# Performance work log

Hardware: AMD Instinct MI355X
Metric: run time of the kernel (lower is better)

The kernel has to match this reference:

```python
import jax, jax.numpy as jnp
import numpy as np


def setup_inputs() -> dict:
    key = jax.random.key(0)
    ks = jax.random.split(key, 12)
    B, T, S, H, I = 32, 32, 400, 1024, 1024
    s = 0.02  # weight init scale
    return {
        "input_": jax.random.normal(ks[0], (B, T, I), jnp.float32),
        "h0": jax.random.normal(ks[1], (B, H), jnp.float32),
        "c0": jax.random.normal(ks[2], (B, H), jnp.float32),
        "h_attn0": jax.random.normal(ks[3], (B, H), jnp.float32),
        "encoder_hy": jax.random.normal(ks[4], (S, B, H), jnp.float32),
        "past_attn": jax.random.uniform(ks[5], (B, S), jnp.float32),
        "W_ih": jax.random.normal(ks[6], (4 * H, I + H), jnp.float32) * s,
        "W_hh": jax.random.normal(ks[7], (4 * H, H), jnp.float32) * s,
        "b_ih": jnp.zeros((4 * H,), jnp.float32),
        "b_hh": jnp.zeros((4 * H,), jnp.float32),
        "W_attn": jax.random.normal(ks[8], (H, H), jnp.float32) * s,
        "W_out": jax.random.normal(ks[9], (H, 2 * H), jnp.float32) * s,
    }


def _decode(input_, h0, c0, h_attn0, encoder_hy, W_ih, W_hh, b_ih, b_hh, W_attn, W_out):
    # encoder_hy: [S, B, H] -> enhy: [B, S, H]
    enhy = jnp.transpose(encoder_hy, (1, 0, 2))
    # attn_in(enhy) is time-invariant (linear, fixed enhy): hoist out of the loop
    enhy_new = jnp.einsum("bsh,gh->bsg", enhy, W_attn)  # [B, S, H]
    xs = jnp.transpose(input_, (1, 0, 2))  # [T, B, I] (batch_first)

    def step(carry, x_k):
        h, c, h_attn = carry
        x = jnp.concatenate([x_k, h_attn], axis=1)  # [B, I+H]
        gates = x @ W_ih.T + b_ih + h @ W_hh.T + b_hh  # [B, 4H]
        i, f, g, o = jnp.split(gates, 4, axis=1)  # torch LSTMCell gate order
        i = jax.nn.sigmoid(i)
        f = jax.nn.sigmoid(f)
        g = jnp.tanh(g)
        o = jax.nn.sigmoid(o)
        c = f * c + i * g
        h = o * jnp.tanh(c)
        # luong_general: attn = bmm(attn_in(enhy), dehy)
        attn = jax.nn.softmax(jnp.einsum("bsh,bh->bs", enhy_new, h), axis=1)
        ctx = jnp.einsum("bs,bsh->bh", attn, enhy)
        h_attn = jnp.tanh(jnp.concatenate([ctx, h], axis=1) @ W_out.T)
        return (h, c, h_attn), (h_attn, attn)

    (h, c, h_attn), (outs, attns) = jax.lax.scan(step, (h0, c0, h_attn0), xs)
    output = jnp.transpose(outs, (1, 0, 2))  # [B, T, H] (batch_first)
    return output, h, c, h_attn, attns  # attns: [T, B, S]


def reference(input_, h0, c0, h_attn0, encoder_hy, past_attn,
              W_ih, W_hh, b_ih, b_hh, W_attn, W_out):
    output, h, c, h_attn, out_attn = _decode(
        input_, h0, c0, h_attn0, encoder_hy, W_ih, W_hh, b_ih, b_hh, W_attn, W_out)
    # coverage='none': past_attn passes through unchanged; loss_cv stays 0.0
    return output, h, c, h_attn, out_attn, past_attn, jnp.float32(0.0)
```

## Files before the change

kernel.cpp:

```cpp
#include <hip/hip_runtime.h>
#include <hip/hip_bf16.h>

using u16 = unsigned short;
typedef __attribute__((ext_vector_type(8))) short bf16x8;
typedef __attribute__((ext_vector_type(4))) float f32x4;
typedef __attribute__((ext_vector_type(4))) u16 u16x4;


__device__ __forceinline__ float bf2f(u16 u){ union{unsigned int i; float f;} v; v.i = ((unsigned int)u)<<16; return v.f; }
__device__ __forceinline__ u16 f2bf(float f){ __hip_bfloat16 h = __float2bfloat16(f); return *reinterpret_cast<u16*>(&h); }
struct HL { u16 h, l; };
__device__ __forceinline__ HL split1(float f){
  HL r; r.h = f2bf(f); r.l = f2bf(f - bf2f(r.h)); return r;
}
__device__ __forceinline__ f32x4 mfma16(bf16x8 a, bf16x8 b, f32x4 c){ return __builtin_amdgcn_mfma_f32_16x16x32_bf16(a,b,c,0,0,0); }


__global__ __launch_bounds__(256) void cast_wih_k(const float* __restrict__ Wih,
    u16* __restrict__ Wxh, u16* __restrict__ Wxl, u16* __restrict__ Wrh, u16* __restrict__ Wrl){
  int v = blockIdx.x*256 + threadIdx.x;
  if (v >= (4096*2048)/4) return;
  int flat = v*4; int j = flat >> 11; int k = flat & 2047;
  float4 f = *(const float4*)(Wih + flat);
  HL s0 = split1(f.x), s1 = split1(f.y), s2 = split1(f.z), s3 = split1(f.w);
  u16x4 h, l;
  h[0]=s0.h; h[1]=s1.h; h[2]=s2.h; h[3]=s3.h;
  l[0]=s0.l; l[1]=s1.l; l[2]=s2.l; l[3]=s3.l;
  if (k < 1024){
    *(u16x4*)(Wxh + (size_t)j*1024 + k) = h;
    *(u16x4*)(Wxl + (size_t)j*1024 + k) = l;
  } else {
    *(u16x4*)(Wrh + (size_t)j*2048 + (k-1024)) = h;
    *(u16x4*)(Wrl + (size_t)j*2048 + (k-1024)) = l;
  }
}

__global__ __launch_bounds__(256) void cast_whh_k(const float* __restrict__ Whh,
    u16* __restrict__ Wrh, u16* __restrict__ Wrl){
  int v = blockIdx.x*256 + threadIdx.x;
  if (v >= (4096*1024)/4) return;
  int flat = v*4; int j = flat >> 10; int k = flat & 1023;
  float4 f = *(const float4*)(Whh + flat);
  HL s0 = split1(f.x), s1 = split1(f.y), s2 = split1(f.z), s3 = split1(f.w);
  u16x4 h, l;
  h[0]=s0.h; h[1]=s1.h; h[2]=s2.h; h[3]=s3.h;
  l[0]=s0.l; l[1]=s1.l; l[2]=s2.l; l[3]=s3.l;
  *(u16x4*)(Wrh + (size_t)j*2048 + 1024 + k) = h;
  *(u16x4*)(Wrl + (size_t)j*2048 + 1024 + k) = l;
}

__global__ __launch_bounds__(256) void cast_split_k(const float* __restrict__ src,
    u16* __restrict__ dh, u16* __restrict__ dl, int n4){
  int v = blockIdx.x*256 + threadIdx.x;
  if (v >= n4) return;
  float4 f = *(const float4*)(src + (size_t)v*4);
  HL s0 = split1(f.x), s1 = split1(f.y), s2 = split1(f.z), s3 = split1(f.w);
  u16x4 h, l;
  h[0]=s0.h; h[1]=s1.h; h[2]=s2.h; h[3]=s3.h;
  l[0]=s0.l; l[1]=s1.l; l[2]=s2.l; l[3]=s3.l;
  *(u16x4*)(dh + (size_t)v*4) = h;
  *(u16x4*)(dl + (size_t)v*4) = l;
}

__global__ __launch_bounds__(256) void cast_x_k(const float* __restrict__ inp,
    u16* __restrict__ Xh, u16* __restrict__ Xl){
  int v = blockIdx.x*256 + threadIdx.x;
  if (v >= (1024*1024)/4) return;
  int flat = v*4; int m = flat >> 10; int k = flat & 1023;
  int t = m >> 5, b = m & 31;
  float4 f = *(const float4*)(inp + ((size_t)(b*32 + t) << 10) + k);
  HL s0 = split1(f.x), s1 = split1(f.y), s2 = split1(f.z), s3 = split1(f.w);
  u16x4 h, l;
  h[0]=s0.h; h[1]=s1.h; h[2]=s2.h; h[3]=s3.h;
  l[0]=s0.l; l[1]=s1.l; l[2]=s2.l; l[3]=s3.l;
  *(u16x4*)(Xh + flat) = h;
  *(u16x4*)(Xl + flat) = l;
}

__global__ __launch_bounds__(256) void watsplit_k(const float* __restrict__ Wattn,
    u16* __restrict__ Wth, u16* __restrict__ Wtl){
  __shared__ float t[32][33];
  int gx = blockIdx.x, cx = blockIdx.y;
  int ty = threadIdx.x >> 5, tx = threadIdx.x & 31;
  #pragma unroll
  for (int i=0;i<4;++i){
    int g = gx*32 + ty + i*8;
    t[ty+i*8][tx] = Wattn[(size_t)g*1024 + cx*32 + tx];
  }
  __syncthreads();
  #pragma unroll
  for (int i=0;i<4;++i){
    int c = cx*32 + ty + i*8;
    HL s = split1(t[tx][ty+i*8]);
    Wth[(size_t)c*1024 + gx*32 + tx] = s.h;
    Wtl[(size_t)c*1024 + gx*32 + tx] = s.l;
  }
}

__global__ __launch_bounds__(256) void cast_encb_k(const float* __restrict__ enc,
    u16* __restrict__ encb){
  int v = blockIdx.x*256 + threadIdx.x;
  if (v >= (400*32*1024)/8) return;
  size_t flat = (size_t)v*8;
  int c = flat & 1023; int rem = flat >> 10;
  int b = rem & 31, s = rem >> 5;
  float4 f0 = *(const float4*)(enc + flat);
  float4 f1 = *(const float4*)(enc + flat + 4);
  u16x4 h0, h1;
  h0[0]=f2bf(f0.x); h0[1]=f2bf(f0.y); h0[2]=f2bf(f0.z); h0[3]=f2bf(f0.w);
  h1[0]=f2bf(f1.x); h1[1]=f2bf(f1.y); h1[2]=f2bf(f1.z); h1[3]=f2bf(f1.w);
  u16* dst = encb + ((size_t)b*400 + s)*1024 + c;
  *(u16x4*)dst = h0;
  *(u16x4*)(dst+4) = h1;
}

__global__ __launch_bounds__(256) void init_misc_k(const float* __restrict__ h0, const float* __restrict__ c0,
    const float* __restrict__ ha0, const float* __restrict__ past,
    u16* __restrict__ Zh0, u16* __restrict__ Zl0, float* __restrict__ cbuf,
    float* __restrict__ out_past, float* __restrict__ out_loss){
  int idx = blockIdx.x*256 + threadIdx.x;
  if (idx < 65536){
    int b = idx >> 11, col = idx & 2047;
    float v = (col < 1024) ? ha0[b*1024 + col] : h0[b*1024 + col - 1024];
    HL s = split1(v);
    Zh0[idx] = s.h; Zl0[idx] = s.l;
  } else if (idx < 65536 + 32768){
    int i = idx - 65536; cbuf[i] = c0[i];
  } else if (idx < 65536 + 32768 + 12800){
    int i = idx - 98304; out_past[i] = past[i];
  } else if (idx == 65536 + 32768 + 12800){
    out_loss[0] = 0.f;
  }
}

__global__ __launch_bounds__(256) void gemm128_bias_k(
    const u16* __restrict__ Ah, const u16* __restrict__ Al,
    const u16* __restrict__ Bh, const u16* __restrict__ Bl, float* __restrict__ C,
    const float* __restrict__ bias0, const float* __restrict__ bias1, int M, int N, int K)
{
  __shared__ __align__(16) u16 Ash[4096], Asl[4096], Bsh[4096], Bsl[4096];
  const int tid = threadIdx.x;
  const int lane = tid & 63, w = tid >> 6;
  const int wm = w >> 1, wn = w & 1;
  const int m0 = blockIdx.y * 128, n0 = blockIdx.x * 128;
  const int r = lane & 15, q = lane >> 4;

  f32x4 acc[4][4];
  #pragma unroll
  for (int i=0;i<4;i++)
    #pragma unroll
    for (int j=0;j<4;j++) acc[i][j] = (f32x4){0.f,0.f,0.f,0.f};

  const int NT = K >> 5;
  const int srow = tid >> 2;
  const int skp  = (tid & 3) * 8;
  bf16x8 rah0, rah1, ral0, ral1, rbh0, rbh1, rbl0, rbl1;

  {
    size_t ao = (size_t)(m0 + srow) * K + skp;
    size_t bo = (size_t)(n0 + srow) * K + skp;
    rah0 = *(const bf16x8*)(Ah + ao);  rah1 = *(const bf16x8*)(Ah + ao + (size_t)64*K);
    ral0 = *(const bf16x8*)(Al + ao);  ral1 = *(const bf16x8*)(Al + ao + (size_t)64*K);
    rbh0 = *(const bf16x8*)(Bh + bo);  rbh1 = *(const bf16x8*)(Bh + bo + (size_t)64*K);
    rbl0 = *(const bf16x8*)(Bl + bo);  rbl1 = *(const bf16x8*)(Bl + bo + (size_t)64*K);
  }

  for (int kt = 0; kt < NT; ++kt){
    __syncthreads();
    *(bf16x8*)(Ash + tid*8)        = rah0;
    *(bf16x8*)(Ash + 2048 + tid*8) = rah1;
    *(bf16x8*)(Asl + tid*8)        = ral0;
    *(bf16x8*)(Asl + 2048 + tid*8) = ral1;
    *(bf16x8*)(Bsh + tid*8)        = rbh0;
    *(bf16x8*)(Bsh + 2048 + tid*8) = rbh1;
    *(bf16x8*)(Bsl + tid*8)        = rbl0;
    *(bf16x8*)(Bsl + 2048 + tid*8) = rbl1;
    __syncthreads();
    if (kt + 1 < NT){
      size_t ao = (size_t)(m0 + srow) * K + (kt+1)*32 + skp;
      size_t bo = (size_t)(n0 + srow) * K + (kt+1)*32 + skp;
      rah0 = *(const bf16x8*)(Ah + ao);  rah1 = *(const bf16x8*)(Ah + ao + (size_t)64*K);
      ral0 = *(const bf16x8*)(Al + ao);  ral1 = *(const bf16x8*)(Al + ao + (size_t)64*K);
      rbh0 = *(const bf16x8*)(Bh + bo);  rbh1 = *(const bf16x8*)(Bh + bo + (size_t)64*K);
      rbl0 = *(const bf16x8*)(Bl + bo);  rbl1 = *(const bf16x8*)(Bl + bo + (size_t)64*K);
    }
    bf16x8 afh[4], afl[4], bfh[4], bfl[4];
    #pragma unroll
    for (int mf=0; mf<4; ++mf){
      int off = (wm*64 + mf*16 + r)*32 + q*8;
      afh[mf] = *(const bf16x8*)(Ash + off);
      afl[mf] = *(const bf16x8*)(Asl + off);
    }
    #pragma unroll
    for (int nf=0; nf<4; ++nf){
      int off = (wn*64 + nf*16 + r)*32 + q*8;
      bfh[nf] = *(const bf16x8*)(Bsh + off);
      bfl[nf] = *(const bf16x8*)(Bsl + off);
    }
    #pragma unroll
    for (int mf=0; mf<4; ++mf)
      #pragma unroll
      for (int nf=0; nf<4; ++nf){
        acc[mf][nf] = mfma16(afh[mf], bfh[nf], acc[mf][nf]);
        acc[mf][nf] = mfma16(afh[mf], bfl[nf], acc[mf][nf]);
        acc[mf][nf] = mfma16(afl[mf], bfh[nf], acc[mf][nf]);
      }
  }

  #pragma unroll
  for (int mf=0; mf<4; ++mf)
    #pragma unroll
    for (int nf=0; nf<4; ++nf)
      #pragma unroll
      for (int rr=0; rr<4; ++rr){
        int row = m0 + wm*64 + mf*16 + q*4 + rr;
        int col = n0 + wn*64 + nf*16 + r;
        C[(size_t)row*N + col] = acc[mf][nf][rr] + bias0[col] + bias1[col];
      }
}


__global__ __launch_bounds__(512) void rec_cell_k(
    const u16* __restrict__ Zh, const u16* __restrict__ Zl,
    const u16* __restrict__ Wh, const u16* __restrict__ Wl,
    const float* __restrict__ gX, float* __restrict__ cbuf,
    u16* __restrict__ Znh, u16* __restrict__ Znl,
    u16* __restrict__ Zoh, u16* __restrict__ Zol,
    float* __restrict__ out_h, float* __restrict__ out_c, int last)
{
  __shared__ float red[8][512];
  __shared__ float gsum[512];
  const int tid = threadIdx.x, lane = tid & 63, w = tid >> 6;
  const int j4 = blockIdx.x;
  const int r = lane & 15, q = lane >> 4;
  const int k0 = w*256;

  f32x4 acc0 = (f32x4){0,0,0,0}, acc1 = (f32x4){0,0,0,0};
  const size_t aoff = (size_t)r*2048 + k0 + q*8;
  const size_t boff = (size_t)((r>>2)*1024 + j4*4 + (r&3))*2048 + k0 + q*8;
  #pragma unroll
  for (int kt = 0; kt < 8; ++kt){
    bf16x8 a0h = *(const bf16x8*)(Zh + aoff + kt*32);
    bf16x8 a0l = *(const bf16x8*)(Zl + aoff + kt*32);
    bf16x8 a1h = *(const bf16x8*)(Zh + aoff + (size_t)16*2048 + kt*32);
    bf16x8 a1l = *(const bf16x8*)(Zl + aoff + (size_t)16*2048 + kt*32);
    bf16x8 bh  = *(const bf16x8*)(Wh + boff + kt*32);
    bf16x8 bl  = *(const bf16x8*)(Wl + boff + kt*32);
    acc0 = mfma16(a0h, bh, acc0);
    acc0 = mfma16(a0h, bl, acc0);
    acc0 = mfma16(a0l, bh, acc0);
    acc1 = mfma16(a1h, bh, acc1);
    acc1 = mfma16(a1h, bl, acc1);
    acc1 = mfma16(a1l, bh, acc1);
  }
  #pragma unroll
  for (int rr=0; rr<4; ++rr){
    red[w][(q*4+rr)*16 + r]        = acc0[rr];
    red[w][256 + (q*4+rr)*16 + r]  = acc1[rr];
  }
  __syncthreads();
  {
    float v = 0.f;
    #pragma unroll
    for (int w2=0; w2<8; ++w2) v += red[w2][tid];
    gsum[tid] = v;
  }
  __syncthreads();
  if (tid < 128){
    int b = tid >> 2, c = tid & 3;
    int j = j4*4 + c;
    float gs[4];
    #pragma unroll
    for (int g=0; g<4; ++g)
      gs[g] = gsum[b*16 + g*4 + c] + gX[(size_t)b*4096 + g*1024 + j];
    int idx = b*1024 + j;
    float iv = 1.f/(1.f + expf(-gs[0]));
    float fv = 1.f/(1.f + expf(-gs[1]));
    float gv = tanhf(gs[2]);
    float ov = 1.f/(1.f + expf(-gs[3]));
    float cn = fv * cbuf[idx] + iv*gv;
    cbuf[idx] = cn;
    float h = ov * tanhf(cn);
    HL s = split1(h);
    size_t zi = (size_t)b*2048 + 1024 + j;
    Znh[zi] = s.h; Znl[zi] = s.l;
    Zoh[zi] = s.h; Zol[zi] = s.l;
    if (last){ out_h[idx] = h; out_c[idx] = cn; }
  }
}

__global__ __launch_bounds__(512) void u_mfma_k(
    const u16* __restrict__ Zoh, const u16* __restrict__ Zol,
    const u16* __restrict__ Wth, const u16* __restrict__ Wtl,
    float* __restrict__ ubuf)
{
  __shared__ float red[8][512];
  const int tid = threadIdx.x, lane = tid & 63, w = tid >> 6;
  const int cc = blockIdx.x;
  const int r = lane & 15, q = lane >> 4;
  f32x4 acc0 = (f32x4){0,0,0,0}, acc1 = (f32x4){0,0,0,0};
  const size_t aoff = (size_t)r*2048 + 1024 + w*128 + q*8;
  const size_t boff = (size_t)(cc*16 + r)*1024 + w*128 + q*8;
  #pragma unroll
  for (int kt=0; kt<4; ++kt){
    bf16x8 a0h = *(const bf16x8*)(Zoh + aoff + kt*32);
    bf16x8 a0l = *(const bf16x8*)(Zol + aoff + kt*32);
    bf16x8 a1h = *(const bf16x8*)(Zoh + aoff + (size_t)16*2048 + kt*32);
    bf16x8 a1l = *(const bf16x8*)(Zol + aoff + (size_t)16*2048 + kt*32);
    bf16x8 bh  = *(const bf16x8*)(Wth + boff + kt*32);
    bf16x8 bl  = *(const bf16x8*)(Wtl + boff + kt*32);
    acc0 = mfma16(a0h, bh, acc0);
    acc0 = mfma16(a0h, bl, acc0);
    acc0 = mfma16(a0l, bh, acc0);
    acc1 = mfma16(a1h, bh, acc1);
    acc1 = mfma16(a1h, bl, acc1);
    acc1 = mfma16(a1l, bh, acc1);
  }
  #pragma unroll
  for (int rr=0; rr<4; ++rr){
    red[w][(q*4+rr)*16 + r]      = acc0[rr];
    red[w][(16 + q*4+rr)*16 + r] = acc1[rr];
  }
  __syncthreads();
  {
    int b = tid >> 4, jj = tid & 15;
    float v = 0.f;
    #pragma unroll
    for (int w2=0; w2<8; ++w2) v += red[w2][tid];
    ubuf[(size_t)b*1024 + cc*16 + jj] = v;
  }
}

__global__ __launch_bounds__(512) void flash_bf16_k(const u16* __restrict__ encb,
    const float* __restrict__ ubuf, float* __restrict__ scbuf,
    float* __restrict__ ctxp, float* __restrict__ mlbuf)
{
  __shared__ float wacc[8][1024];
  __shared__ float wml[16];
  const int tid = threadIdx.x, lane = tid & 63, w = tid >> 6;
  const int b = blockIdx.x >> 4, sc16 = blockIdx.x & 15;
  const int s0 = sc16 * 25;

  const float* up = ubuf + (size_t)b*1024 + lane*16;
  float uu[16];
  #pragma unroll
  for (int i=0;i<4;i++){ float4 t4 = *(const float4*)(up + i*4); uu[4*i]=t4.x; uu[4*i+1]=t4.y; uu[4*i+2]=t4.z; uu[4*i+3]=t4.w; }

  float m = -1e30f, l = 0.f;
  float acc[16];
  #pragma unroll
  for (int i=0;i<16;i++) acc[i] = 0.f;

  for (int s = s0 + w; s < s0 + 25; s += 8){
    const u16* ep = encb + ((size_t)b*400 + s)*1024 + lane*16;
    bf16x8 e0 = *(const bf16x8*)ep;
    bf16x8 e1 = *(const bf16x8*)(ep + 8);
    float er[16];
    #pragma unroll
    for (int i=0;i<8;i++){ er[i] = bf2f((u16)e0[i]); er[8+i] = bf2f((u16)e1[i]); }
    float sc = 0.f;
    #pragma unroll
    for (int i=0;i<16;i++) sc = fmaf(er[i], uu[i], sc);
    #pragma unroll
    for (int off=32; off; off>>=1) sc += __shfl_xor(sc, off);
    if (lane == 0) scbuf[(size_t)b*400 + s] = sc;
    if (sc > m){
      float f = expf(m - sc);
      l *= f;
      #pragma unroll
      for (int i=0;i<16;i++) acc[i] *= f;
      m = sc;
    }
    float wgt = expf(sc - m);
    l += wgt;
    #pragma unroll
    for (int i=0;i<16;i++) acc[i] = fmaf(wgt, er[i], acc[i]);
  }

  #pragma unroll
  for (int i=0;i<16;i++) wacc[w][lane*16+i] = acc[i];
  if (lane == 0){ wml[w*2] = m; wml[w*2+1] = l; }
  __syncthreads();

  float M = wml[0];
  #pragma unroll
  for (int i=1;i<8;i++) M = fmaxf(M, wml[i*2]);
  float c0v = 0.f, c1v = 0.f;
  #pragma unroll
  for (int i=0;i<8;i++){
    float f = expf(wml[i*2] - M);
    c0v = fmaf(wacc[i][tid],       f, c0v);
    c1v = fmaf(wacc[i][tid + 512], f, c1v);
  }
  size_t co = ((size_t)b*16 + sc16)*1024;
  ctxp[co + tid]       = c0v;
  ctxp[co + tid + 512] = c1v;
  if (tid == 0){
    float L = 0.f;
    #pragma unroll
    for (int i=0;i<8;i++) L += wml[i*2+1] * expf(wml[i*2] - M);
    mlbuf[((size_t)b*16 + sc16)*2]     = M;
    mlbuf[((size_t)b*16 + sc16)*2 + 1] = L;
  }
}

__global__ __launch_bounds__(512) void flash_f32_k(const float* __restrict__ enc,
    const float* __restrict__ ubuf, float* __restrict__ scbuf,
    float* __restrict__ ctxp, float* __restrict__ mlbuf)
{
  __shared__ float wacc[8][1024];
  __shared__ float wml[16];
  const int tid = threadIdx.x, lane = tid & 63, w = tid >> 6;
  const int b = blockIdx.x >> 4, sc16 = blockIdx.x & 15;
  const int s0 = sc16 * 25;

  const float* up = ubuf + (size_t)b*1024 + lane*16;
  float uu[16];
  #pragma unroll
  for (int i=0;i<4;i++){ float4 t4 = *(const float4*)(up + i*4); uu[4*i]=t4.x; uu[4*i+1]=t4.y; uu[4*i+2]=t4.z; uu[4*i+3]=t4.w; }

  float m = -1e30f, l = 0.f;
  float acc[16];
  #pragma unroll
  for (int i=0;i<16;i++) acc[i] = 0.f;

  for (int s = s0 + w; s < s0 + 25; s += 8){
    const float* ep = enc + ((size_t)s*32 + b)*1024 + lane*16;
    float er[16];
    #pragma unroll
    for (int i=0;i<4;i++){ float4 e4 = *(const float4*)(ep + i*4); er[4*i]=e4.x; er[4*i+1]=e4.y; er[4*i+2]=e4.z; er[4*i+3]=e4.w; }
    float sc = 0.f;
    #pragma unroll
    for (int i=0;i<16;i++) sc = fmaf(er[i], uu[i], sc);
    #pragma unroll
    for (int off=32; off; off>>=1) sc += __shfl_xor(sc, off);
    if (lane == 0) scbuf[(size_t)b*400 + s] = sc;
    if (sc > m){
      float f = expf(m - sc);
      l *= f;
      #pragma unroll
      for (int i=0;i<16;i++) acc[i] *= f;
      m = sc;
    }
    float wgt = expf(sc - m);
    l += wgt;
    #pragma unroll
    for (int i=0;i<16;i++) acc[i] = fmaf(wgt, er[i], acc[i]);
  }

  #pragma unroll
  for (int i=0;i<16;i++) wacc[w][lane*16+i] = acc[i];
  if (lane == 0){ wml[w*2] = m; wml[w*2+1] = l; }
  __syncthreads();

  float M = wml[0];
  #pragma unroll
  for (int i=1;i<8;i++) M = fmaxf(M, wml[i*2]);
  float c0v = 0.f, c1v = 0.f;
  #pragma unroll
  for (int i=0;i<8;i++){
    float f = expf(wml[i*2] - M);
    c0v = fmaf(wacc[i][tid],       f, c0v);
    c1v = fmaf(wacc[i][tid + 512], f, c1v);
  }
  size_t co = ((size_t)b*16 + sc16)*1024;
  ctxp[co + tid]       = c0v;
  ctxp[co + tid + 512] = c1v;
  if (tid == 0){
    float L = 0.f;
    #pragma unroll
    for (int i=0;i<8;i++) L += wml[i*2+1] * expf(wml[i*2] - M);
    mlbuf[((size_t)b*16 + sc16)*2]     = M;
    mlbuf[((size_t)b*16 + sc16)*2 + 1] = L;
  }
}

__global__ __launch_bounds__(256) void combine_k(const float* __restrict__ scbuf,
    const float* __restrict__ ctxp, const float* __restrict__ mlbuf,
    u16* __restrict__ Zoh, u16* __restrict__ Zol, float* __restrict__ attn_out)
{
  const int b = blockIdx.x >> 3, cc = blockIdx.x & 7;
  const int tid = threadIdx.x;
  float M = -1e30f;
  #pragma unroll
  for (int i=0;i<16;i++) M = fmaxf(M, mlbuf[((size_t)b*16 + i)*2]);
  float L = 0.f;
  #pragma unroll
  for (int i=0;i<16;i++) L += mlbuf[((size_t)b*16 + i)*2 + 1] * expf(mlbuf[((size_t)b*16 + i)*2] - M);
  float invL = 1.f / L;
  if (tid < 128){
    int col = cc*128 + tid;
    float v = 0.f;
    #pragma unroll
    for (int i=0;i<16;i++)
      v = fmaf(ctxp[((size_t)b*16 + i)*1024 + col], expf(mlbuf[((size_t)b*16 + i)*2] - M), v);
    HL s = split1(v * invL);
    size_t zi = (size_t)b*2048 + col;
    Zoh[zi] = s.h; Zol[zi] = s.l;
  } else if (tid < 128 + 50){
    int s = cc*50 + (tid - 128);
    attn_out[(size_t)b*400 + s] = expf(scbuf[(size_t)b*400 + s] - M) * invL;
  }
}

__global__ __launch_bounds__(512) void outg_fused_k(
    const u16* __restrict__ Zoh, const u16* __restrict__ Zol,
    const u16* __restrict__ Woh, const u16* __restrict__ Wol,
    float* __restrict__ out_outp , u16* __restrict__ Znh, u16* __restrict__ Znl,
    float* __restrict__ out_hattn, int last)
{
  __shared__ float red[8][256];
  const int tid = threadIdx.x, lane = tid & 63, w = tid >> 6;
  const int ub = blockIdx.x & 63, bh = blockIdx.x >> 6;
  const int r = lane & 15, q = lane >> 4;
  const int k0 = w*256;
  f32x4 acc0 = (f32x4){0,0,0,0};
  const size_t aoff = (size_t)(bh*16 + r)*2048 + k0 + q*8;
  const size_t boff = (size_t)(ub*16 + r)*2048 + k0 + q*8;
  #pragma unroll
  for (int kt=0; kt<8; ++kt){
    bf16x8 ah = *(const bf16x8*)(Zoh + aoff + kt*32);
    bf16x8 al = *(const bf16x8*)(Zol + aoff + kt*32);
    bf16x8 bh_ = *(const bf16x8*)(Woh + boff + kt*32);
    bf16x8 bl_ = *(const bf16x8*)(Wol + boff + kt*32);
    acc0 = mfma16(ah, bh_, acc0);
    acc0 = mfma16(ah, bl_, acc0);
    acc0 = mfma16(al, bh_, acc0);
  }
  #pragma unroll
  for (int rr=0; rr<4; ++rr)
    red[w][(q*4+rr)*16 + r] = acc0[rr];
  __syncthreads();
  if (tid < 256){
    int bloc = tid >> 4, jj = tid & 15;
    float z = 0.f;
    #pragma unroll
    for (int w2=0; w2<8; ++w2) z += red[w2][tid];
    int b = bh*16 + bloc;
    int u = ub*16 + jj;
    float ha = tanhf(z);
    out_outp[(size_t)b*32768 + u] = ha;
    HL s = split1(ha);
    Znh[(size_t)b*2048 + u] = s.h;
    Znl[(size_t)b*2048 + u] = s.l;
    if (last) out_hattn[(size_t)b*1024 + u] = ha;
  }
}


extern "C" void kernel_launch(void* const* d_in, const int* in_sizes, int n_in,
                              void* d_out, int out_size, void* d_ws, size_t ws_size,
                              hipStream_t stream)
{
  const float* input_ = (const float*)d_in[0];
  const float* h0     = (const float*)d_in[1];
  const float* c0     = (const float*)d_in[2];
  const float* ha0    = (const float*)d_in[3];
  const float* enc    = (const float*)d_in[4];
  const float* past   = (const float*)d_in[5];
  const float* W_ih   = (const float*)d_in[6];
  const float* W_hh   = (const float*)d_in[7];
  const float* b_ih   = (const float*)d_in[8];
  const float* b_hh   = (const float*)d_in[9];
  const float* W_attn = (const float*)d_in[10];
  const float* W_out  = (const float*)d_in[11];
  float* out = (float*)d_out;

  const size_t OUT_OUTPUT = 0;
  const size_t OUT_H      = 1048576;
  const size_t OUT_C      = 1081344;
  const size_t OUT_HATTN  = 1114112;
  const size_t OUT_ATTN   = 1146880;
  const size_t OUT_PAST   = 1556480;
  const size_t OUT_LOSS   = 1569280;

  const size_t OFF_WRH   = 0;
  const size_t OFF_WRL   = 16777216;
  const size_t OFF_WXH   = 33554432;
  const size_t OFF_WXL   = 41943040;
  const size_t OFF_WOH   = 50331648;
  const size_t OFF_WOL   = 54525952;
  const size_t OFF_XBH   = 58720256;
  const size_t OFF_XBL   = 60817408;
  const size_t OFF_GATEX = 62914560;
  const size_t OFF_ZBH   = 79691776;
  const size_t OFF_ZBL   = 79953920;
  const size_t OFF_ZOH   = 80216064;
  const size_t OFF_ZOL   = 80347136;
  const size_t OFF_CBUF  = 80478208;
  const size_t OFF_UBUF  = 80609280;
  const size_t OFF_SC    = 80740352;
  const size_t WS_NEED   = 82939904;
  if (ws_size < WS_NEED) return;

  const size_t OFF_ENCB  = WS_NEED;
  const size_t WS_BIG    = WS_NEED + 26214400;
  const bool use_bf16enc = (ws_size >= WS_BIG);

  const size_t OFF_CTXP  = OFF_WXH;
  const size_t OFF_ML    = OFF_WXH + 2097152;

  char* ws = (char*)d_ws;
  u16*   Wrh   = (u16*)(ws + OFF_WRH);
  u16*   Wrl   = (u16*)(ws + OFF_WRL);
  u16*   Wxh   = (u16*)(ws + OFF_WXH);
  u16*   Wxl   = (u16*)(ws + OFF_WXL);
  u16*   Woh   = (u16*)(ws + OFF_WOH);
  u16*   Wol   = (u16*)(ws + OFF_WOL);
  u16*   Xbh   = (u16*)(ws + OFF_XBH);
  u16*   Xbl   = (u16*)(ws + OFF_XBL);
  u16*   Wth   = (u16*)(ws + OFF_XBH);
  u16*   Wtl   = (u16*)(ws + OFF_XBL);
  float* gateX = (float*)(ws + OFF_GATEX);
  u16*   Zbh   = (u16*)(ws + OFF_ZBH);
  u16*   Zbl   = (u16*)(ws + OFF_ZBL);
  u16*   Zoh   = (u16*)(ws + OFF_ZOH);
  u16*   Zol   = (u16*)(ws + OFF_ZOL);
  float* cbuf  = (float*)(ws + OFF_CBUF);
  float* ubuf  = (float*)(ws + OFF_UBUF);
  float* sc    = (float*)(ws + OFF_SC);
  float* ctxp  = (float*)(ws + OFF_CTXP);
  float* mlbuf = (float*)(ws + OFF_ML);
  u16*   encb  = (u16*)(ws + OFF_ENCB);

  cast_wih_k <<<8192, 256, 0, stream>>>(W_ih, Wxh, Wxl, Wrh, Wrl);
  cast_whh_k <<<4096, 256, 0, stream>>>(W_hh, Wrh, Wrl);
  cast_split_k<<<2048, 256, 0, stream>>>(W_out, Woh, Wol, (1024*2048)/4);
  cast_x_k   <<<1024, 256, 0, stream>>>(input_, Xbh, Xbl);
  init_misc_k<<<435, 256, 0, stream>>>(h0, c0, ha0, past, Zbh, Zbl, cbuf, out + OUT_PAST, out + OUT_LOSS);
  if (use_bf16enc)
    cast_encb_k<<<6400, 256, 0, stream>>>(enc, encb);

  gemm128_bias_k<<<dim3(32, 8), 256, 0, stream>>>(Xbh, Xbl, Wxh, Wxl, gateX, b_ih, b_hh, 1024, 4096, 1024);
  watsplit_k<<<dim3(32, 32), 256, 0, stream>>>(W_attn, Wth, Wtl);

  for (int t = 0; t < 32; ++t){
    int p = t & 1;
    u16* Zih = Zbh + (size_t)p * 65536;
    u16* Zil = Zbl + (size_t)p * 65536;
    u16* Znh = Zbh + (size_t)(1-p) * 65536;
    u16* Znl = Zbl + (size_t)(1-p) * 65536;
    int last = (t == 31);
    rec_cell_k<<<256, 512, 0, stream>>>(Zih, Zil, Wrh, Wrl,
        gateX + (size_t)t*131072, cbuf, Znh, Znl, Zoh, Zol,
        out + OUT_H, out + OUT_C, last);
    u_mfma_k<<<64, 512, 0, stream>>>(Zoh, Zol, Wth, Wtl, ubuf);
    if (use_bf16enc)
      flash_bf16_k<<<512, 512, 0, stream>>>(encb, ubuf, sc, ctxp, mlbuf);
    else
      flash_f32_k<<<512, 512, 0, stream>>>(enc, ubuf, sc, ctxp, mlbuf);
    combine_k<<<256, 256, 0, stream>>>(sc, ctxp, mlbuf, Zoh, Zol,
        out + OUT_ATTN + (size_t)t*12800);
    outg_fused_k<<<128, 512, 0, stream>>>(Zoh, Zol, Woh, Wol,
        out + OUT_OUTPUT + (size_t)t*1024, Znh, Znl, out + OUT_HATTN, last);
  }
}
```

Measured before the change: 1.400 ms.

## Fuse setup casts into one kernel and widen grids of recurrent step kernels

The six setup cast and init kernels become a single block-dispatched kernel, which removes launch overhead. rec_cell_k now covers 2 hidden units per block with 512 blocks, and u_mfma_k splits the batch across 128 blocks, so each serial per-step kernel exposes more parallelism. The flash kernels drop the online-softmax loop: each wave loads all of its encoder rows up front, batches the shuffle reductions, and computes max and exp once. The change also adds occupancy hints to launch bounds, at the cost of more register pressure and some duplicated A-operand loads.

```diff
diff --git a/kernel.cpp b/kernel.cpp
--- a/kernel.cpp
+++ b/kernel.cpp
@@ -15,66 +15,94 @@
 }
 __device__ __forceinline__ f32x4 mfma16(bf16x8 a, bf16x8 b, f32x4 c){ return __builtin_amdgcn_mfma_f32_16x16x32_bf16(a,b,c,0,0,0); }
 
-
-__global__ __launch_bounds__(256) void cast_wih_k(const float* __restrict__ Wih,
-    u16* __restrict__ Wxh, u16* __restrict__ Wxl, u16* __restrict__ Wrh, u16* __restrict__ Wrl){
-  int v = blockIdx.x*256 + threadIdx.x;
-  if (v >= (4096*2048)/4) return;
-  int flat = v*4; int j = flat >> 11; int k = flat & 2047;
-  float4 f = *(const float4*)(Wih + flat);
-  HL s0 = split1(f.x), s1 = split1(f.y), s2 = split1(f.z), s3 = split1(f.w);
-  u16x4 h, l;
-  h[0]=s0.h; h[1]=s1.h; h[2]=s2.h; h[3]=s3.h;
-  l[0]=s0.l; l[1]=s1.l; l[2]=s2.l; l[3]=s3.l;
-  if (k < 1024){
-    *(u16x4*)(Wxh + (size_t)j*1024 + k) = h;
-    *(u16x4*)(Wxl + (size_t)j*1024 + k) = l;
+__global__ __launch_bounds__(256) void cast_all_k(
+    const float* __restrict__ Wih, const float* __restrict__ Whh,
+    const float* __restrict__ Wout_f, const float* __restrict__ inp,
+    const float* __restrict__ h0, const float* __restrict__ c0,
+    const float* __restrict__ ha0, const float* __restrict__ past,
+    const float* __restrict__ enc,
+    u16* __restrict__ Wxh, u16* __restrict__ Wxl, u16* __restrict__ Wrh, u16* __restrict__ Wrl,
+    u16* __restrict__ Woh, u16* __restrict__ Wol,
+    u16* __restrict__ Xh, u16* __restrict__ Xl,
+    u16* __restrict__ Zh0, u16* __restrict__ Zl0, float* __restrict__ cbuf,
+    float* __restrict__ out_past, float* __restrict__ out_loss,
+    u16* __restrict__ encb, int do_encb)
+{
+  const int blk = blockIdx.x;
+  if (blk < 8192){
+    int v = blk*256 + threadIdx.x;
+    int flat = v*4; int j = flat >> 11; int k = flat & 2047;
+    float4 f = *(const float4*)(Wih + flat);
+    HL s0 = split1(f.x), s1 = split1(f.y), s2 = split1(f.z), s3 = split1(f.w);
+    u16x4 h, l;
+    h[0]=s0.h; h[1]=s1.h; h[2]=s2.h; h[3]=s3.h;
+    l[0]=s0.l; l[1]=s1.l; l[2]=s2.l; l[3]=s3.l;
+    if (k < 1024){
+      *(u16x4*)(Wxh + (size_t)j*1024 + k) = h;
+      *(u16x4*)(Wxl + (size_t)j*1024 + k) = l;
+    } else {
+      *(u16x4*)(Wrh + (size_t)j*2048 + (k-1024)) = h;
+      *(u16x4*)(Wrl + (size_t)j*2048 + (k-1024)) = l;
+    }
+  } else if (blk < 12288){
+    int v = (blk-8192)*256 + threadIdx.x;
+    int flat = v*4; int j = flat >> 10; int k = flat & 1023;
+    float4 f = *(const float4*)(Whh + flat);
+    HL s0 = split1(f.x), s1 = split1(f.y), s2 = split1(f.z), s3 = split1(f.w);
+    u16x4 h, l;
+    h[0]=s0.h; h[1]=s1.h; h[2]=s2.h; h[3]=s3.h;
+    l[0]=s0.l; l[1]=s1.l; l[2]=s2.l; l[3]=s3.l;
+    *(u16x4*)(Wrh + (size_t)j*2048 + 1024 + k) = h;
+    *(u16x4*)(Wrl + (size_t)j*2048 + 1024 + k) = l;
+  } else if (blk < 14336){
+    int v = (blk-12288)*256 + threadIdx.x;
+    float4 f = *(const float4*)(Wout_f + (size_t)v*4);
+    HL s0 = split1(f.x), s1 = split1(f.y), s2 = split1(f.z), s3 = split1(f.w);
+    u16x4 h, l;
+    h[0]=s0.h; h[1]=s1.h; h[2]=s2.h; h[3]=s3.h;
+    l[0]=s0.l; l[1]=s1.l; l[2]=s2.l; l[3]=s3.l;
+    *(u16x4*)(Woh + (size_t)v*4) = h;
+    *(u16x4*)(Wol + (size_t)v*4) = l;
+  } else if (blk < 15360){
+    int v = (blk-14336)*256 + threadIdx.x;
+    int flat = v*4; int m = flat >> 10; int k = flat & 1023;
+    int t = m >> 5, b = m & 31;
+    float4 f = *(const float4*)(inp + ((size_t)(b*32 + t) << 10) + k);
+    HL s0 = split1(f.x), s1 = split1(f.y), s2 = split1(f.z), s3 = split1(f.w);
+    u16x4 h, l;
+    h[0]=s0.h; h[1]=s1.h; h[2]=s2.h; h[3]=s3.h;
+    l[0]=s0.l; l[1]=s1.l; l[2]=s2.l; l[3]=s3.l;
+    *(u16x4*)(Xh + flat) = h;
+    *(u16x4*)(Xl + flat) = l;
+  } else if (blk < 15795){
+    int idx = (blk-15360)*256 + threadIdx.x;
+    if (idx < 65536){
+      int b = idx >> 11, col = idx & 2047;
+      float v = (col < 1024) ? ha0[b*1024 + col] : h0[b*1024 + col - 1024];
+      HL s = split1(v);
+      Zh0[idx] = s.h; Zl0[idx] = s.l;
+    } else if (idx < 65536 + 32768){
+      int i = idx - 65536; cbuf[i] = c0[i];
+    } else if (idx < 65536 + 32768 + 12800){
+      int i = idx - 98304; out_past[i] = past[i];
+    } else if (idx == 65536 + 32768 + 12800){
+      out_loss[0] = 0.f;
+    }
   } else {
-    *(u16x4*)(Wrh + (size_t)j*2048 + (k-1024)) = h;
-    *(u16x4*)(Wrl + (size_t)j*2048 + (k-1024)) = l;
-  }
-}
-
-__global__ __launch_bounds__(256) void cast_whh_k(const float* __restrict__ Whh,
-    u16* __restrict__ Wrh, u16* __restrict__ Wrl){
-  int v = blockIdx.x*256 + threadIdx.x;
-  if (v >= (4096*1024)/4) return;
-  int flat = v*4; int j = flat >> 10; int k = flat & 1023;
-  float4 f = *(const float4*)(Whh + flat);
-  HL s0 = split1(f.x), s1 = split1(f.y), s2 = split1(f.z), s3 = split1(f.w);
-  u16x4 h, l;
-  h[0]=s0.h; h[1]=s1.h; h[2]=s2.h; h[3]=s3.h;
-  l[0]=s0.l; l[1]=s1.l; l[2]=s2.l; l[3]=s3.l;
-  *(u16x4*)(Wrh + (size_t)j*2048 + 1024 + k) = h;
-  *(u16x4*)(Wrl + (size_t)j*2048 + 1024 + k) = l;
-}
-
-__global__ __launch_bounds__(256) void cast_split_k(const float* __restrict__ src,
-    u16* __restrict__ dh, u16* __restrict__ dl, int n4){
-  int v = blockIdx.x*256 + threadIdx.x;
-  if (v >= n4) return;
-  float4 f = *(const float4*)(src + (size_t)v*4);
-  HL s0 = split1(f.x), s1 = split1(f.y), s2 = split1(f.z), s3 = split1(f.w);
-  u16x4 h, l;
-  h[0]=s0.h; h[1]=s1.h; h[2]=s2.h; h[3]=s3.h;
-  l[0]=s0.l; l[1]=s1.l; l[2]=s2.l; l[3]=s3.l;
-  *(u16x4*)(dh + (size_t)v*4) = h;
-  *(u16x4*)(dl + (size_t)v*4) = l;
-}
-
-__global__ __launch_bounds__(256) void cast_x_k(const float* __restrict__ inp,
-    u16* __restrict__ Xh, u16* __restrict__ Xl){
-  int v = blockIdx.x*256 + threadIdx.x;
-  if (v >= (1024*1024)/4) return;
-  int flat = v*4; int m = flat >> 10; int k = flat & 1023;
-  int t = m >> 5, b = m & 31;
-  float4 f = *(const float4*)(inp + ((size_t)(b*32 + t) << 10) + k);
-  HL s0 = split1(f.x), s1 = split1(f.y), s2 = split1(f.z), s3 = split1(f.w);
-  u16x4 h, l;
-  h[0]=s0.h; h[1]=s1.h; h[2]=s2.h; h[3]=s3.h;
-  l[0]=s0.l; l[1]=s1.l; l[2]=s2.l; l[3]=s3.l;
-  *(u16x4*)(Xh + flat) = h;
-  *(u16x4*)(Xl + flat) = l;
+    if (!do_encb) return;
+    int v = (blk-15795)*256 + threadIdx.x;
+    size_t flat = (size_t)v*8;
+    int c = flat & 1023; int rem = flat >> 10;
+    int b = rem & 31, s = rem >> 5;
+    float4 f0 = *(const float4*)(enc + flat);
+    float4 f1 = *(const float4*)(enc + flat + 4);
+    u16x4 h0v, h1v;
+    h0v[0]=f2bf(f0.x); h0v[1]=f2bf(f0.y); h0v[2]=f2bf(f0.z); h0v[3]=f2bf(f0.w);
+    h1v[0]=f2bf(f1.x); h1v[1]=f2bf(f1.y); h1v[2]=f2bf(f1.z); h1v[3]=f2bf(f1.w);
+    u16* dst = encb + ((size_t)b*400 + s)*1024 + c;
+    *(u16x4*)dst = h0v;
+    *(u16x4*)(dst+4) = h1v;
+  }
 }
 
 __global__ __launch_bounds__(256) void watsplit_k(const float* __restrict__ Wattn,
@@ -94,42 +122,6 @@
     HL s = split1(t[tx][ty+i*8]);
     Wth[(size_t)c*1024 + gx*32 + tx] = s.h;
     Wtl[(size_t)c*1024 + gx*32 + tx] = s.l;
-  }
-}
-
-__global__ __launch_bounds__(256) void cast_encb_k(const float* __restrict__ enc,
-    u16* __restrict__ encb){
-  int v = blockIdx.x*256 + threadIdx.x;
-  if (v >= (400*32*1024)/8) return;
-  size_t flat = (size_t)v*8;
-  int c = flat & 1023; int rem = flat >> 10;
-  int b = rem & 31, s = rem >> 5;
-  float4 f0 = *(const float4*)(enc + flat);
-  float4 f1 = *(const float4*)(enc + flat + 4);
-  u16x4 h0, h1;
-  h0[0]=f2bf(f0.x); h0[1]=f2bf(f0.y); h0[2]=f2bf(f0.z); h0[3]=f2bf(f0.w);
-  h1[0]=f2bf(f1.x); h1[1]=f2bf(f1.y); h1[2]=f2bf(f1.z); h1[3]=f2bf(f1.w);
-  u16* dst = encb + ((size_t)b*400 + s)*1024 + c;
-  *(u16x4*)dst = h0;
-  *(u16x4*)(dst+4) = h1;
-}
-
-__global__ __launch_bounds__(256) void init_misc_k(const float* __restrict__ h0, const float* __restrict__ c0,
-    const float* __restrict__ ha0, const float* __restrict__ past,
-    u16* __restrict__ Zh0, u16* __restrict__ Zl0, float* __restrict__ cbuf,
-    float* __restrict__ out_past, float* __restrict__ out_loss){
-  int idx = blockIdx.x*256 + threadIdx.x;
-  if (idx < 65536){
-    int b = idx >> 11, col = idx & 2047;
-    float v = (col < 1024) ? ha0[b*1024 + col] : h0[b*1024 + col - 1024];
-    HL s = split1(v);
-    Zh0[idx] = s.h; Zl0[idx] = s.l;
-  } else if (idx < 65536 + 32768){
-    int i = idx - 65536; cbuf[i] = c0[i];
-  } else if (idx < 65536 + 32768 + 12800){
-    int i = idx - 98304; out_past[i] = past[i];
-  } else if (idx == 65536 + 32768 + 12800){
-    out_loss[0] = 0.f;
   }
 }
 
@@ -220,7 +212,7 @@
 }
 
 
-__global__ __launch_bounds__(512) void rec_cell_k(
+__global__ __launch_bounds__(512, 4) void rec_cell_k(
     const u16* __restrict__ Zh, const u16* __restrict__ Zl,
     const u16* __restrict__ Wh, const u16* __restrict__ Wl,
     const float* __restrict__ gX, float* __restrict__ cbuf,
@@ -231,13 +223,13 @@
   __shared__ float red[8][512];
   __shared__ float gsum[512];
   const int tid = threadIdx.x, lane = tid & 63, w = tid >> 6;
-  const int j4 = blockIdx.x;
+  const int j2 = blockIdx.x;
   const int r = lane & 15, q = lane >> 4;
   const int k0 = w*256;
 
   f32x4 acc0 = (f32x4){0,0,0,0}, acc1 = (f32x4){0,0,0,0};
   const size_t aoff = (size_t)r*2048 + k0 + q*8;
-  const size_t boff = (size_t)((r>>2)*1024 + j4*4 + (r&3))*2048 + k0 + q*8;
+  const size_t boff = (size_t)((r>>2)*1024 + j2*2 + (r&1))*2048 + k0 + q*8;
   #pragma unroll
   for (int kt = 0; kt < 8; ++kt){
     bf16x8 a0h = *(const bf16x8*)(Zh + aoff + kt*32);
@@ -266,9 +258,9 @@
     gsum[tid] = v;
   }
   __syncthreads();
-  if (tid < 128){
-    int b = tid >> 2, c = tid & 3;
-    int j = j4*4 + c;
+  if (tid < 64){
+    int b = tid >> 1, c = tid & 1;
+    int j = j2*2 + c;
     float gs[4];
     #pragma unroll
     for (int g=0; g<4; ++g)
@@ -294,44 +286,37 @@
     const u16* __restrict__ Wth, const u16* __restrict__ Wtl,
     float* __restrict__ ubuf)
 {
-  __shared__ float red[8][512];
+  __shared__ float red[8][256];
   const int tid = threadIdx.x, lane = tid & 63, w = tid >> 6;
-  const int cc = blockIdx.x;
+  const int cc = blockIdx.x & 63, bh = blockIdx.x >> 6;
   const int r = lane & 15, q = lane >> 4;
-  f32x4 acc0 = (f32x4){0,0,0,0}, acc1 = (f32x4){0,0,0,0};
-  const size_t aoff = (size_t)r*2048 + 1024 + w*128 + q*8;
+  f32x4 acc0 = (f32x4){0,0,0,0};
+  const size_t aoff = (size_t)(bh*16 + r)*2048 + 1024 + w*128 + q*8;
   const size_t boff = (size_t)(cc*16 + r)*1024 + w*128 + q*8;
   #pragma unroll
   for (int kt=0; kt<4; ++kt){
-    bf16x8 a0h = *(const bf16x8*)(Zoh + aoff + kt*32);
-    bf16x8 a0l = *(const bf16x8*)(Zol + aoff + kt*32);
-    bf16x8 a1h = *(const bf16x8*)(Zoh + aoff + (size_t)16*2048 + kt*32);
-    bf16x8 a1l = *(const bf16x8*)(Zol + aoff + (size_t)16*2048 + kt*32);
-    bf16x8 bh  = *(const bf16x8*)(Wth + boff + kt*32);
-    bf16x8 bl  = *(const bf16x8*)(Wtl + boff + kt*32);
-    acc0 = mfma16(a0h, bh, acc0);
-    acc0 = mfma16(a0h, bl, acc0);
-    acc0 = mfma16(a0l, bh, acc0);
-    acc1 = mfma16(a1h, bh, acc1);
-    acc1 = mfma16(a1h, bl, acc1);
-    acc1 = mfma16(a1l, bh, acc1);
-  }
-  #pragma unroll
-  for (int rr=0; rr<4; ++rr){
-    red[w][(q*4+rr)*16 + r]      = acc0[rr];
-    red[w][(16 + q*4+rr)*16 + r] = acc1[rr];
-  }
+    bf16x8 ah = *(const bf16x8*)(Zoh + aoff + kt*32);
+    bf16x8 al = *(const bf16x8*)(Zol + aoff + kt*32);
+    bf16x8 bh_ = *(const bf16x8*)(Wth + boff + kt*32);
+    bf16x8 bl_ = *(const bf16x8*)(Wtl + boff + kt*32);
+    acc0 = mfma16(ah, bh_, acc0);
+    acc0 = mfma16(ah, bl_, acc0);
+    acc0 = mfma16(al, bh_, acc0);
+  }
+  #pragma unroll
+  for (int rr=0; rr<4; ++rr)
+    red[w][(q*4+rr)*16 + r] = acc0[rr];
   __syncthreads();
-  {
-    int b = tid >> 4, jj = tid & 15;
+  if (tid < 256){
+    int bloc = tid >> 4, jj = tid & 15;
     float v = 0.f;
     #pragma unroll
     for (int w2=0; w2<8; ++w2) v += red[w2][tid];
-    ubuf[(size_t)b*1024 + cc*16 + jj] = v;
-  }
-}
-
-__global__ __launch_bounds__(512) void flash_bf16_k(const u16* __restrict__ encb,
+    ubuf[(size_t)(bh*16 + bloc)*1024 + cc*16 + jj] = v;
+  }
+}
+
+__global__ __launch_bounds__(512, 4) void flash_bf16_k(const u16* __restrict__ encb,
     const float* __restrict__ ubuf, float* __restrict__ scbuf,
     float* __restrict__ ctxp, float* __restrict__ mlbuf)
 {
@@ -346,39 +331,61 @@
   #pragma unroll
   for (int i=0;i<4;i++){ float4 t4 = *(const float4*)(up + i*4); uu[4*i]=t4.x; uu[4*i+1]=t4.y; uu[4*i+2]=t4.z; uu[4*i+3]=t4.w; }
 
-  float m = -1e30f, l = 0.f;
+  const int nr = (w == 0) ? 4 : 3;
+  bf16x8 e0[4], e1[4];
+  #pragma unroll
+  for (int i=0;i<4;++i){
+    if (i < nr){
+      const u16* ep = encb + ((size_t)b*400 + s0 + w + 8*i)*1024 + lane*16;
+      e0[i] = *(const bf16x8*)ep;
+      e1[i] = *(const bf16x8*)(ep + 8);
+    }
+  }
+  float scv[4];
+  #pragma unroll
+  for (int i=0;i<4;++i){
+    if (i < nr){
+      float sc = 0.f;
+      #pragma unroll
+      for (int j=0;j<8;j++) sc = fmaf(bf2f((u16)e0[i][j]), uu[j], sc);
+      #pragma unroll
+      for (int j=0;j<8;j++) sc = fmaf(bf2f((u16)e1[i][j]), uu[8+j], sc);
+      scv[i] = sc;
+    } else scv[i] = -1e30f;
+  }
+  #pragma unroll
+  for (int off=32; off; off>>=1){
+    #pragma unroll
+    for (int i=0;i<4;++i) scv[i] += (i < nr) ? __shfl_xor(scv[i], off) : 0.f;
+  }
+  #pragma unroll
+  for (int i=0;i<4;++i)
+    if (i < nr && lane == 0) scbuf[(size_t)b*400 + s0 + w + 8*i] = scv[i];
+
+  float m = scv[0];
+  #pragma unroll
+  for (int i=1;i<4;++i) if (i < nr) m = fmaxf(m, scv[i]);
+  float wt[4]; float l = 0.f;
+  #pragma unroll
+  for (int i=0;i<4;++i){
+    wt[i] = (i < nr) ? expf(scv[i] - m) : 0.f;
+    l += wt[i];
+  }
   float acc[16];
   #pragma unroll
-  for (int i=0;i<16;i++) acc[i] = 0.f;
-
-  for (int s = s0 + w; s < s0 + 25; s += 8){
-    const u16* ep = encb + ((size_t)b*400 + s)*1024 + lane*16;
-    bf16x8 e0 = *(const bf16x8*)ep;
-    bf16x8 e1 = *(const bf16x8*)(ep + 8);
-    float er[16];
-    #pragma unroll
-    for (int i=0;i<8;i++){ er[i] = bf2f((u16)e0[i]); er[8+i] = bf2f((u16)e1[i]); }
-    float sc = 0.f;
-    #pragma unroll
-    for (int i=0;i<16;i++) sc = fmaf(er[i], uu[i], sc);
-    #pragma unroll
-    for (int off=32; off; off>>=1) sc += __shfl_xor(sc, off);
-    if (lane == 0) scbuf[(size_t)b*400 + s] = sc;
-    if (sc > m){
-      float f = expf(m - sc);
-      l *= f;
-      #pragma unroll
-      for (int i=0;i<16;i++) acc[i] *= f;
-      m = sc;
-    }
-    float wgt = expf(sc - m);
-    l += wgt;
-    #pragma unroll
-    for (int i=0;i<16;i++) acc[i] = fmaf(wgt, er[i], acc[i]);
-  }
-
-  #pragma unroll
-  for (int i=0;i<16;i++) wacc[w][lane*16+i] = acc[i];
+  for (int j=0;j<16;j++) acc[j] = 0.f;
+  #pragma unroll
+  for (int i=0;i<4;++i){
+    if (i < nr){
+      #pragma unroll
+      for (int j=0;j<8;j++)  acc[j]   = fmaf(wt[i], bf2f((u16)e0[i][j]), acc[j]);
+      #pragma unroll
+      for (int j=0;j<8;j++)  acc[8+j] = fmaf(wt[i], bf2f((u16)e1[i][j]), acc[8+j]);
+    }
+  }
+
+  #pragma unroll
+  for (int j=0;j<16;j++) wacc[w][lane*16+j] = acc[j];
   if (lane == 0){ wml[w*2] = m; wml[w*2+1] = l; }
   __syncthreads();
 
@@ -404,7 +411,7 @@
   }
 }
 
-__global__ __launch_bounds__(512) void flash_f32_k(const float* __restrict__ enc,
+__global__ __launch_bounds__(512, 4) void flash_f32_k(const float* __restrict__ enc,
     const float* __restrict__ ubuf, float* __restrict__ scbuf,
     float* __restrict__ ctxp, float* __restrict__ mlbuf)
 {
@@ -419,37 +426,60 @@
   #pragma unroll
   for (int i=0;i<4;i++){ float4 t4 = *(const float4*)(up + i*4); uu[4*i]=t4.x; uu[4*i+1]=t4.y; uu[4*i+2]=t4.z; uu[4*i+3]=t4.w; }
 
-  float m = -1e30f, l = 0.f;
+  const int nr = (w == 0) ? 4 : 3;
+  float er[4][16];
+  #pragma unroll
+  for (int i=0;i<4;++i){
+    if (i < nr){
+      const float* ep = enc + ((size_t)(s0 + w + 8*i)*32 + b)*1024 + lane*16;
+      #pragma unroll
+      for (int jj=0;jj<4;jj++){
+        float4 e4 = *(const float4*)(ep + jj*4);
+        er[i][4*jj]=e4.x; er[i][4*jj+1]=e4.y; er[i][4*jj+2]=e4.z; er[i][4*jj+3]=e4.w;
+      }
+    }
+  }
+  float scv[4];
+  #pragma unroll
+  for (int i=0;i<4;++i){
+    if (i < nr){
+      float sc = 0.f;
+      #pragma unroll
+      for (int j=0;j<16;j++) sc = fmaf(er[i][j], uu[j], sc);
+      scv[i] = sc;
+    } else scv[i] = -1e30f;
+  }
+  #pragma unroll
+  for (int off=32; off; off>>=1){
+    #pragma unroll
+    for (int i=0;i<4;++i) scv[i] += (i < nr) ? __shfl_xor(scv[i], off) : 0.f;
+  }
+  #pragma unroll
+  for (int i=0;i<4;++i)
+    if (i < nr && lane == 0) scbuf[(size_t)b*400 + s0 + w + 8*i] = scv[i];
+
+  float m = scv[0];
+  #pragma unroll
+  for (int i=1;i<4;++i) if (i < nr) m = fmaxf(m, scv[i]);
+  float wt[4]; float l = 0.f;
+  #pragma unroll
+  for (int i=0;i<4;++i){
+    wt[i] = (i < nr) ? expf(scv[i] - m) : 0.f;
+    l += wt[i];
+  }
   float acc[16];
   #pragma unroll
-  for (int i=0;i<16;i++) acc[i] = 0.f;
-
-  for (int s = s0 + w; s < s0 + 25; s += 8){
-    const float* ep = enc + ((size_t)s*32 + b)*1024 + lane*16;
-    float er[16];
-    #pragma unroll
-    for (int i=0;i<4;i++){ float4 e4 = *(const float4*)(ep + i*4); er[4*i]=e4.x; er[4*i+1]=e4.y; er[4*i+2]=e4.z; er[4*i+3]=e4.w; }
-    float sc = 0.f;
-    #pragma unroll
-    for (int i=0;i<16;i++) sc = fmaf(er[i], uu[i], sc);
-    #pragma unroll
-    for (int off=32; off; off>>=1) sc += __shfl_xor(sc, off);
-    if (lane == 0) scbuf[(size_t)b*400 + s] = sc;
-    if (sc > m){
-      float f = expf(m - sc);
-      l *= f;
-      #pragma unroll
-      for (int i=0;i<16;i++) acc[i] *= f;
-      m = sc;
-    }
-    float wgt = expf(sc - m);
-    l += wgt;
-    #pragma unroll
-    for (int i=0;i<16;i++) acc[i] = fmaf(wgt, er[i], acc[i]);
-  }
-
-  #pragma unroll
-  for (int i=0;i<16;i++) wacc[w][lane*16+i] = acc[i];
+  for (int j=0;j<16;j++) acc[j] = 0.f;
+  #pragma unroll
+  for (int i=0;i<4;++i){
+    if (i < nr){
+      #pragma unroll
+      for (int j=0;j<16;j++) acc[j] = fmaf(wt[i], er[i][j], acc[j]);
+    }
+  }
+
+  #pragma unroll
+  for (int j=0;j<16;j++) wacc[w][lane*16+j] = acc[j];
   if (lane == 0){ wml[w*2] = m; wml[w*2+1] = l; }
   __syncthreads();
 
@@ -623,13 +653,11 @@
   float* mlbuf = (float*)(ws + OFF_ML);
   u16*   encb  = (u16*)(ws + OFF_ENCB);
 
-  cast_wih_k <<<8192, 256, 0, stream>>>(W_ih, Wxh, Wxl, Wrh, Wrl);
-  cast_whh_k <<<4096, 256, 0, stream>>>(W_hh, Wrh, Wrl);
-  cast_split_k<<<2048, 256, 0, stream>>>(W_out, Woh, Wol, (1024*2048)/4);
-  cast_x_k   <<<1024, 256, 0, stream>>>(input_, Xbh, Xbl);
-  init_misc_k<<<435, 256, 0, stream>>>(h0, c0, ha0, past, Zbh, Zbl, cbuf, out + OUT_PAST, out + OUT_LOSS);
-  if (use_bf16enc)
-    cast_encb_k<<<6400, 256, 0, stream>>>(enc, encb);
+  cast_all_k<<<22195, 256, 0, stream>>>(W_ih, W_hh, W_out, input_,
+      h0, c0, ha0, past, enc,
+      Wxh, Wxl, Wrh, Wrl, Woh, Wol, Xbh, Xbl,
+      Zbh, Zbl, cbuf, out + OUT_PAST, out + OUT_LOSS,
+      encb, use_bf16enc ? 1 : 0);
 
   gemm128_bias_k<<<dim3(32, 8), 256, 0, stream>>>(Xbh, Xbl, Wxh, Wxl, gateX, b_ih, b_hh, 1024, 4096, 1024);
   watsplit_k<<<dim3(32, 32), 256, 0, stream>>>(W_attn, Wth, Wtl);
@@ -641,10 +669,10 @@
     u16* Znh = Zbh + (size_t)(1-p) * 65536;
     u16* Znl = Zbl + (size_t)(1-p) * 65536;
     int last = (t == 31);
-    rec_cell_k<<<256, 512, 0, stream>>>(Zih, Zil, Wrh, Wrl,
+    rec_cell_k<<<512, 512, 0, stream>>>(Zih, Zil, Wrh, Wrl,
         gateX + (size_t)t*131072, cbuf, Znh, Znl, Zoh, Zol,
         out + OUT_H, out + OUT_C, last);
-    u_mfma_k<<<64, 512, 0, stream>>>(Zoh, Zol, Wth, Wtl, ubuf);
+    u_mfma_k<<<128, 512, 0, stream>>>(Zoh, Zol, Wth, Wtl, ubuf);
     if (use_bf16enc)
       flash_bf16_k<<<512, 512, 0, stream>>>(encb, ubuf, sc, ctxp, mlbuf);
     else
```

After: 1.583 ms. 13.0% more time.
